# Kernel tuning notes

Hardware: AMD Instinct MI355X
Metric: run time of the kernel (lower is better)

## Reference

```python
import jax, jax.numpy as jnp
import jax.scipy.linalg as jsl
import numpy as np

B, T, C = 2, 4096, 1024
HK = HV = 8           # linear_num_key_heads == linear_num_value_heads
DK = DV = 128         # linear_key_head_dim / linear_value_head_dim
CHUNK = 64
CONV_K = 4
KEY_DIM = HK * DK
VAL_DIM = HV * DV
CONV_DIM = 2 * KEY_DIM + VAL_DIM
EPS = 1e-6


def setup_inputs() -> dict:
    key = jax.random.key(0)
    ks = jax.random.split(key, 8)
    s = 0.02
    x = jax.random.normal(ks[0], (B, T, C), jnp.float32)
    W_qkvz = jax.random.normal(ks[1], (C, 2 * KEY_DIM + 2 * VAL_DIM), jnp.float32) * s
    W_ba = jax.random.normal(ks[2], (C, 2 * HV), jnp.float32) * s
    conv_w = jax.random.normal(ks[3], (CONV_DIM, 1, CONV_K), jnp.float32) * 0.3  # depthwise (O,1,K)
    dt_bias = jnp.ones((HV,), jnp.float32)
    A_log = jnp.log(jax.random.uniform(ks[4], (HV,), jnp.float32, 0.5, 8.0))
    norm_weight = jnp.ones((DV,), jnp.float32)
    W_out = jax.random.normal(ks[5], (VAL_DIM, C), jnp.float32) * s
    return {"x": x, "W_qkvz": W_qkvz, "W_ba": W_ba, "conv_w": conv_w,
            "dt_bias": dt_bias, "A_log": A_log, "norm_weight": norm_weight, "W_out": W_out}


def _l2norm(x, eps=EPS):
    return x * jax.lax.rsqrt(jnp.sum(x * x, -1, keepdims=True) + eps)


def _chunk_gated_delta_rule(q, k, v, g, beta, chunk=CHUNK):
    # q,k: (B,T,H,DK); v: (B,T,H,DV); g,beta: (B,T,H)
    q = _l2norm(q)
    k = _l2norm(k)
    tr = lambda x: jnp.swapaxes(x, 1, 2).astype(jnp.float32)  # -> (B,H,T,...)
    q, k, v, g, beta = tr(q), tr(k), tr(v), tr(g), tr(beta)
    b, h, t, dk = k.shape
    dv = v.shape[-1]
    n = t // chunk  # T divisible by chunk (pad_size == 0)
    q = q * (dk ** -0.5)
    v_beta = v * beta[..., None]
    k_beta = k * beta[..., None]
    rs = lambda x: x.reshape(b, h, n, chunk, x.shape[-1])
    q, k, v_beta, k_beta = rs(q), rs(k), rs(v_beta), rs(k_beta)
    g = jnp.cumsum(g.reshape(b, h, n, chunk), axis=-1)
    # decay_mask[..., i, j] = exp(g_i - g_j) for j <= i, else 0
    decay = jnp.tril(jnp.exp(jnp.tril(g[..., :, None] - g[..., None, :])))
    # forward substitution == unit-lower-triangular solve: (I + tri)^{-1}
    tri = jnp.tril(jnp.einsum('bhnck,bhndk->bhncd', k_beta, k) * decay, -1)
    eye = jnp.eye(chunk, dtype=jnp.float32)
    Tm = jsl.solve_triangular(eye + tri, jnp.broadcast_to(eye, tri.shape), lower=True)
    v_new = Tm @ v_beta                                   # (B,H,N,C,DV)
    k_cum = Tm @ (k_beta * jnp.exp(g)[..., None])         # (B,H,N,C,DK)
    keep_low = jnp.tril(jnp.ones((chunk, chunk), bool))

    def step(S, inp):
        q_i, k_i, v_i, kc_i, g_i, dm_i = inp              # (B,H,C,*)
        attn = jnp.where(keep_low, (q_i @ jnp.swapaxes(k_i, -1, -2)) * dm_i, 0.0)
        v_n = v_i - kc_i @ S
        out = (q_i * jnp.exp(g_i)[..., None]) @ S + attn @ v_n
        g_last = g_i[..., -1]
        S = S * jnp.exp(g_last)[..., None, None] + jnp.einsum(
            'bhck,bhcv->bhkv', k_i * jnp.exp(g_last[..., None] - g_i)[..., None], v_n)
        return S, out

    mv = lambda x: jnp.moveaxis(x, 2, 0)                  # chunk axis to front
    S0 = jnp.zeros((b, h, dk, dv), jnp.float32)
    S, outs = jax.lax.scan(step, S0, (mv(q), mv(k), mv(v_new), mv(k_cum), mv(g), mv(decay)))
    out = jnp.moveaxis(outs, 0, 2).reshape(b, h, t, dv)
    return jnp.swapaxes(out, 1, 2), S                     # (B,T,H,DV), (B,H,DK,DV)


def reference(x, W_qkvz, W_ba, conv_w, dt_bias, A_log, norm_weight, W_out):
    Bx, Tx, Cx = x.shape
    ratio = HV // HK
    qkvz = (x @ W_qkvz).reshape(Bx, Tx, HK, 2 * DK + 2 * ratio * DV)
    q, k, v, z = jnp.split(qkvz, [DK, 2 * DK, 2 * DK + ratio * DV], axis=3)
    v = v.reshape(Bx, Tx, HV, DV)
    z = z.reshape(Bx, Tx, HV, DV)
    ba = (x @ W_ba).reshape(Bx, Tx, HK, 2 * ratio)
    b_, a_ = jnp.split(ba, [ratio], axis=3)
    b_ = b_.reshape(Bx, Tx, HV)
    a_ = a_.reshape(Bx, Tx, HV)
    mixed = jnp.concatenate([q.reshape(Bx, Tx, -1), k.reshape(Bx, Tx, -1),
                             v.reshape(Bx, Tx, -1)], axis=-1)
    # causal depthwise conv1d (left pad K-1, take first T)
    xc = jnp.swapaxes(mixed, 1, 2)                        # (B, CONV_DIM, T)
    conv = jax.lax.conv_general_dilated(xc, conv_w, (1,), [(CONV_K - 1, 0)],
                                        dimension_numbers=('NCH', 'OIH', 'NCH'),
                                        feature_group_count=CONV_DIM)
    conv = jnp.swapaxes(jax.nn.silu(conv), 1, 2)          # (B,T,CONV_DIM)
    qc, kc, vc = jnp.split(conv, [KEY_DIM, 2 * KEY_DIM], axis=-1)
    qc = qc.reshape(Bx, Tx, HK, DK)
    kc = kc.reshape(Bx, Tx, HK, DK)
    vc = vc.reshape(Bx, Tx, HV, DV)
    if ratio > 1:
        qc = jnp.repeat(qc, ratio, axis=2)
        kc = jnp.repeat(kc, ratio, axis=2)
    beta = jax.nn.sigmoid(b_)
    g = -jnp.exp(A_log) * jax.nn.softplus(a_ + dt_bias)
    core, _ = _chunk_gated_delta_rule(qc, kc, vc, g, beta)
    # GatedRMSNorm over head_v_dim, gated by silu(z)
    h = core.astype(jnp.float32)
    var = jnp.mean(h * h, -1, keepdims=True)
    h = norm_weight * (h * jax.lax.rsqrt(var + EPS))
    h = h * jax.nn.silu(z.astype(jnp.float32))
    return h.reshape(Bx, Tx, VAL_DIM) @ W_out
```

## Files before the change

kernel.cpp:

```cpp
#include <hip/hip_runtime.h>
#include <cstddef>

#define Bx 2
#define Tn 4096
#define Hh 8

typedef unsigned short u16;
typedef unsigned int u32;
typedef __attribute__((ext_vector_type(8))) short short8;
typedef __attribute__((ext_vector_type(4))) float f32x4;

__device__ __forceinline__ float bf2f(u16 u) {
  u32 x = ((u32)u) << 16;
  return __uint_as_float(x);
}
__device__ __forceinline__ u16 f2bf(float f) {
  u32 x = __float_as_uint(f);
  u32 lsb = (x >> 16) & 1;
  x += 0x7fffu + lsb;
  return (u16)(x >> 16);
}
__device__ __forceinline__ u32 pack2(float a, float b) {
  return (u32)f2bf(a) | ((u32)f2bf(b) << 16);
}
__device__ __forceinline__ short8 cvt8(float4 f0, float4 f1) {
  uint4 p;
  p.x = pack2(f0.x, f0.y);
  p.y = pack2(f0.z, f0.w);
  p.z = pack2(f1.x, f1.y);
  p.w = pack2(f1.z, f1.w);
  return *(short8*)&p;
}
__device__ __forceinline__ void async16(u16* lds, const u16* g) {
  __builtin_amdgcn_global_load_lds((const __attribute__((address_space(1))) void*)g,
                                   (__attribute__((address_space(3))) void*)lds, 16, 0, 0);
}

__global__ __launch_bounds__(256) void conv_bf16(const float* __restrict__ X,
                                                 u16* __restrict__ Xb) {
  int i = (blockIdx.x * 256 + threadIdx.x) * 8;
  float4 v0 = *(const float4*)&X[i];
  float4 v1 = *(const float4*)&X[i + 4];
  uint4 pv;
  pv.x = pack2(v0.x, v0.y);
  pv.y = pack2(v0.z, v0.w);
  pv.z = pack2(v1.x, v1.y);
  pv.w = pack2(v1.z, v1.w);
  *(uint4*)&Xb[i] = pv;
}

__global__ __launch_bounds__(256) void transpose_bf16(const float* __restrict__ W,
                                                      u16* __restrict__ WT,
                                                      int K, int N) {
  __shared__ float tile[64][68];
  int nb = blockIdx.x, kb = blockIdx.y;
  int tid = threadIdx.x;
  int r = tid >> 4, c4 = (tid & 15) * 4;
#pragma unroll
  for (int p = 0; p < 4; p++) {
    int k = kb * 64 + p * 16 + r;
    float4 v = *(const float4*)&W[(size_t)k * N + nb * 64 + c4];
    tile[p * 16 + r][c4] = v.x;
    tile[p * 16 + r][c4 + 1] = v.y;
    tile[p * 16 + r][c4 + 2] = v.z;
    tile[p * 16 + r][c4 + 3] = v.w;
  }
  __syncthreads();
  int rn = tid >> 2, ck = (tid & 3) * 16;
#pragma unroll
  for (int s = 0; s < 2; s++) {
    int k0 = ck + s * 8;
    uint4 pv;
    pv.x = pack2(tile[k0 + 0][rn], tile[k0 + 1][rn]);
    pv.y = pack2(tile[k0 + 2][rn], tile[k0 + 3][rn]);
    pv.z = pack2(tile[k0 + 4][rn], tile[k0 + 5][rn]);
    pv.w = pack2(tile[k0 + 6][rn], tile[k0 + 7][rn]);
    *(uint4*)&WT[(size_t)(nb * 64 + rn) * K + kb * 64 + k0] = pv;
  }
}

template<int EPI>
__global__ __launch_bounds__(256) void gemm_mfma(const u16* __restrict__ A,
                                                 const u16* __restrict__ Bt,
                                                 u16* __restrict__ O1,
                                                 u16* __restrict__ O2,
                                                 float* __restrict__ O3,
                                                 int Nfull) {
  const int K = 1024;
  __shared__ u16 As[128 * 32];
  __shared__ u16 Bs[128 * 32];
  int bn = blockIdx.x, bm = blockIdx.y;
  int tid = threadIdx.x;
  int wave = tid >> 6, lane = tid & 63;
  int wr = wave >> 1, wc = wave & 1;

  f32x4 acc[4][4];
#pragma unroll
  for (int i = 0; i < 4; i++)
#pragma unroll
    for (int j = 0; j < 4; j++) acc[i][j] = (f32x4){0.f, 0.f, 0.f, 0.f};

  const u16* Ab = A + (size_t)(bm * 128 + wave * 32 + (lane >> 2)) * K + (lane & 3) * 8;
  const u16* Bb = Bt + (size_t)(bn * 128 + wave * 32 + (lane >> 2)) * K + (lane & 3) * 8;
  u16* AsW = &As[(wave * 32) * 32];
  u16* BsW = &Bs[(wave * 32) * 32];

  int m_lane = lane & 15, k_lane = (lane >> 4) * 8;
  const u16* arow0 = &As[(wr * 64 + m_lane) * 32 + k_lane];
  const u16* brow0 = &Bs[(wc * 64 + m_lane) * 32 + k_lane];

  for (int kk = 0; kk < K; kk += 32) {
    __syncthreads();
    async16(AsW, Ab + kk);
    async16(AsW + 16 * 32, Ab + 16 * K + kk);
    async16(BsW, Bb + kk);
    async16(BsW + 16 * 32, Bb + 16 * K + kk);
    __syncthreads();
    short8 a[4], b[4];
#pragma unroll
    for (int t = 0; t < 4; t++) a[t] = *(const short8*)(arow0 + t * 16 * 32);
#pragma unroll
    for (int t = 0; t < 4; t++) b[t] = *(const short8*)(brow0 + t * 16 * 32);
#pragma unroll
    for (int i = 0; i < 4; i++)
#pragma unroll
      for (int j = 0; j < 4; j++)
        acc[i][j] = __builtin_amdgcn_mfma_f32_16x16x32_bf16(a[i], b[j], acc[i][j], 0, 0, 0);
  }

  int n0 = bn * 128;
  int cbase = wc * 64 + (lane & 15);
  int rbase = bm * 128 + wr * 64 + ((lane >> 4) * 4);
  if (EPI == 1) {
    int h = n0 >> 9, sub = (n0 >> 7) & 3;
    u16* dst;
    size_t stride;
    if (sub < 3) { dst = O1 + (size_t)(sub * 1024 + h * 128); stride = 3072; }
    else         { dst = O2 + (size_t)(h * 128);              stride = 1024; }
#pragma unroll
    for (int i = 0; i < 4; i++)
#pragma unroll
      for (int j = 0; j < 4; j++)
#pragma unroll
        for (int r = 0; r < 4; r++)
          dst[(size_t)(rbase + i * 16 + r) * stride + cbase + j * 16] = f2bf(acc[i][j][r]);
  } else {
#pragma unroll
    for (int i = 0; i < 4; i++)
#pragma unroll
      for (int j = 0; j < 4; j++)
#pragma unroll
        for (int r = 0; r < 4; r++)
          O3[(size_t)(rbase + i * 16 + r) * Nfull + n0 + cbase + j * 16] = acc[i][j][r];
  }
}

__global__ __launch_bounds__(128) void ba_kernel(const float* __restrict__ x,
                                                 const float* __restrict__ Wba,
                                                 const float* __restrict__ dtb,
                                                 const float* __restrict__ Alog,
                                                 float* __restrict__ betab,
                                                 float* __restrict__ gb) {
  __shared__ float xs[1024];
  __shared__ float part[8][16];
  int row = blockIdx.x, tid = threadIdx.x;
#pragma unroll
  for (int r = 0; r < 2; r++) {
    int f4 = r * 128 + tid;
    *(float4*)&xs[f4 * 4] = *(const float4*)&x[(size_t)row * 1024 + f4 * 4];
  }
  __syncthreads();
  int col = tid & 15, seg = tid >> 4;
  float a = 0.f;
  for (int k = seg * 128; k < seg * 128 + 128; k++) a += xs[k] * Wba[k * 16 + col];
  part[seg][col] = a;
  __syncthreads();
  if (tid < 8) {
    float bval = 0.f, aval = 0.f;
#pragma unroll
    for (int q = 0; q < 8; q++) { bval += part[q][tid * 2]; aval += part[q][tid * 2 + 1]; }
    betab[(size_t)row * 8 + tid] = 1.f / (1.f + expf(-bval));
    float spin = aval + dtb[tid];
    float sp = (spin > 20.f) ? spin : log1pf(expf(spin));
    gb[(size_t)row * 8 + tid] = -expf(Alog[tid]) * sp;
  }
}

__global__ __launch_bounds__(256) void convnorm(const u16* __restrict__ mixed,
                                                const float* __restrict__ cw,
                                                const float* __restrict__ gbuf,
                                                u16* __restrict__ qn,
                                                u16* __restrict__ kn,
                                                u16* __restrict__ kdT) {
  __shared__ __align__(16) u16 sRaw[67 * 128];
  __shared__ __align__(16) u16 sO[64 * 136];
  __shared__ float red_s[256];
  __shared__ float inv_s[64];
  __shared__ float eglc_s[64];
  int n = blockIdx.x, bh = blockIdx.y, type = blockIdx.z;
  int b = bh >> 3, h = bh & 7;
  int t0 = n * 64, tid = threadIdx.x;
  int srow = tid >> 4, scol8 = (tid & 15) * 8;
  int base = type * 1024;

#pragma unroll
  for (int pass = 0; pass < 5; pass++) {
    int r = pass * 16 + srow;
    if (r < 67) {
      int t = t0 - 3 + r;
      uint4 v = make_uint4(0u, 0u, 0u, 0u);
      if (t >= 0) v = *(const uint4*)&mixed[(size_t)(b * Tn + t) * 3072 + base + h * 128 + scol8];
      *(uint4*)&sRaw[r * 128 + scol8] = v;
    }
  }
  if (type == 1 && tid < 64) {
    float gv = gbuf[(size_t)(b * Tn + t0 + tid) * 8 + h];
#pragma unroll
    for (int off = 1; off < 64; off <<= 1) {
      float o = __shfl_up(gv, off, 64);
      if (tid >= off) gv += o;
    }
    float gl = __shfl(gv, 63, 64);
    eglc_s[tid] = expf(gl - gv);
  }
  __syncthreads();

#pragma unroll
  for (int it = 0; it < 32; it++) {
    int idx = it * 256 + tid;
    int i = idx >> 7, d = idx & 127;
    int colw = (base + h * 128 + d) * 4;
    float a = 0.f;
#pragma unroll
    for (int tap = 0; tap < 4; tap++)
      a += bf2f(sRaw[(i + tap) * 128 + d]) * cw[colw + tap];
    a = a / (1.f + expf(-a));
    sO[i * 136 + d] = f2bf(a);
  }
  __syncthreads();
  {
    int i = tid >> 2, p = tid & 3;
    float ss = 0.f;
#pragma unroll
    for (int d = p * 32; d < p * 32 + 32; d += 2) {
      u32 w2 = *(const u32*)&sO[i * 136 + d];
      float a = bf2f(w2 & 0xffff), b2 = bf2f(w2 >> 16);
      ss += a * a + b2 * b2;
    }
    red_s[tid] = ss;
  }
  __syncthreads();
  if (tid < 64) {
    float inv = rsqrtf(red_s[tid * 4] + red_s[tid * 4 + 1] + red_s[tid * 4 + 2] + red_s[tid * 4 + 3] + 1e-6f);
    inv_s[tid] = (type == 0) ? inv * 0.08838834764831845f : inv;
  }
  __syncthreads();
  u16* dstRow = (type == 0 ? qn : kn) + (size_t)(bh * Tn + t0) * 128;
#pragma unroll
  for (int it = 0; it < 16; it++) {
    int idx = it * 256 + tid;
    int i = idx >> 6, d2 = (idx & 63) * 2;
    u32 w2 = *(const u32*)&sO[i * 136 + d2];
    float inv = inv_s[i];
    float q0 = bf2f(w2 & 0xffff) * inv, q1 = bf2f(w2 >> 16) * inv;
    u32 pk = pack2(q0, q1);
    if (type == 1) *(u32*)&sO[i * 136 + d2] = pk;
    *(u32*)&dstRow[(size_t)i * 128 + d2] = pk;
  }
  if (type == 1) {
    __syncthreads();
    const size_t tbase = (size_t)(bh * 64 + n) * 8192;
#pragma unroll
    for (int it = 0; it < 32; it++) {
      int idx = it * 256 + tid;
      int d = idx >> 6, i = idx & 63;
      kdT[tbase + d * 64 + i] = f2bf(bf2f(sO[i * 136 + d]) * eglc_s[i]);
    }
  }
}

__global__ __launch_bounds__(256) void prep(const u16* __restrict__ mixed,
                                            const float* __restrict__ cw,
                                            const float* __restrict__ gbuf,
                                            const float* __restrict__ betabuf,
                                            u16* qbuf,
                                            u16* kbuf,
                                            u16* __restrict__ vnT,
                                            u16* __restrict__ attn,
                                            float* __restrict__ egl) {
  __shared__ __align__(16) u16 sKn[64 * 136];
  __shared__ __align__(16) u16 sQn[64 * 136];
  __shared__ __align__(16) u16 sRawV[67 * 128];
  __shared__ float gc_s[64], egc_s[64], bet_s[64];
  float* triL = (float*)sQn;

  int n = blockIdx.x, bh = blockIdx.y;
  int b = bh >> 3, h = bh & 7;
  int t0 = n * 64;
  int tid = threadIdx.x;
  const int rowg0 = b * Tn + t0;
  const int rowh0 = bh * Tn + t0;
  const size_t tbase = (size_t)(bh * 64 + n) * 8192;

  int wv = tid >> 6, lane = tid & 63;
  int m16 = lane & 15, q8 = (lane >> 4) * 8, qr = (lane >> 4) * 4;
  int srow = tid >> 4, scol8 = (tid & 15) * 8;

#pragma unroll
  for (int it = 0; it < 4; it++) {
    int idx = it * 256 + tid;
    int i = idx >> 4, c8 = (idx & 15) * 8;
    *(uint4*)&sQn[i * 136 + c8] = *(const uint4*)&qbuf[(size_t)(rowh0 + i) * 128 + c8];
    *(uint4*)&sKn[i * 136 + c8] = *(const uint4*)&kbuf[(size_t)(rowh0 + i) * 128 + c8];
  }
#pragma unroll
  for (int pass = 0; pass < 5; pass++) {
    int r = pass * 16 + srow;
    if (r < 67) {
      int t = t0 - 3 + r;
      uint4 v = make_uint4(0u, 0u, 0u, 0u);
      if (t >= 0) v = *(const uint4*)&mixed[(size_t)(b * Tn + t) * 3072 + 2048 + h * 128 + scol8];
      *(uint4*)&sRawV[r * 128 + scol8] = v;
    }
  }
  if (tid < 64) {
    float gv = gbuf[(size_t)(rowg0 + tid) * 8 + h];
    float bv = betabuf[(size_t)(rowg0 + tid) * 8 + h];
#pragma unroll
    for (int off = 1; off < 64; off <<= 1) {
      float o = __shfl_up(gv, off, 64);
      if (tid >= off) gv += o;
    }
    float gl = __shfl(gv, 63, 64);
    gc_s[tid] = gv;
    egc_s[tid] = expf(gv);
    bet_s[tid] = bv;
    if (tid == 63) egl[bh * 64 + n] = expf(gl);
  }
  __syncthreads();

#pragma unroll
  for (int it = 0; it < 16; it++) {
    int idx = it * 256 + tid;
    int i = idx >> 6, d2 = (idx & 63) * 2;
    u32 w2 = *(const u32*)&sQn[i * 136 + d2];
    float e = egc_s[i];
    *(u32*)&qbuf[(size_t)(rowh0 + i) * 128 + d2] =
        pack2(bf2f(w2 & 0xffff) * e, bf2f(w2 >> 16) * e);
  }
  {
    short8 qa[4];
#pragma unroll
    for (int kt = 0; kt < 4; kt++)
      qa[kt] = *(const short8*)&sQn[(wv * 16 + m16) * 136 + kt * 32 + q8];
    u16* atp = attn + (size_t)(bh * 64 + n) * 4096;
#pragma unroll
    for (int jt = 0; jt < 4; jt++) {
      int j = jt * 16 + m16;
      if (jt <= wv) {
        f32x4 o = (f32x4){0.f, 0.f, 0.f, 0.f};
#pragma unroll
        for (int kt = 0; kt < 4; kt++) {
          short8 kb = *(const short8*)&sKn[(jt * 16 + m16) * 136 + kt * 32 + q8];
          o = __builtin_amdgcn_mfma_f32_16x16x32_bf16(qa[kt], kb, o, 0, 0, 0);
        }
#pragma unroll
        for (int r = 0; r < 4; r++) {
          int i = wv * 16 + qr + r;
          float val = (j <= i) ? o[r] * expf(gc_s[i] - gc_s[j]) : 0.f;
          atp[i * 64 + j] = f2bf(val);
        }
      } else {
#pragma unroll
        for (int r = 0; r < 4; r++) atp[(wv * 16 + qr + r) * 64 + j] = 0;
      }
    }
  }
  __syncthreads();
  {
    short8 ka[4];
#pragma unroll
    for (int kt = 0; kt < 4; kt++)
      ka[kt] = *(const short8*)&sKn[(wv * 16 + m16) * 136 + kt * 32 + q8];
#pragma unroll
    for (int jt = 0; jt < 4; jt++) {
      int j = jt * 16 + m16;
      if (jt <= wv) {
        f32x4 o = (f32x4){0.f, 0.f, 0.f, 0.f};
#pragma unroll
        for (int kt = 0; kt < 4; kt++) {
          short8 kb = *(const short8*)&sKn[(jt * 16 + m16) * 136 + kt * 32 + q8];
          o = __builtin_amdgcn_mfma_f32_16x16x32_bf16(ka[kt], kb, o, 0, 0, 0);
        }
#pragma unroll
        for (int r = 0; r < 4; r++) {
          int i = wv * 16 + qr + r;
          triL[i * 64 + j] = (j < i) ? bet_s[i] * expf(gc_s[i] - gc_s[j]) * o[r] : 0.f;
        }
      } else if (jt == wv + 1) {
#pragma unroll
        for (int r = 0; r < 4; r++) triL[(wv * 16 + qr + r) * 64 + j] = 0.f;
      }
    }
  }
  __syncthreads();

  {
    int mat = tid >> 7, c = tid & 127;
    float x[64];
    if (mat == 0) {
#pragma unroll
      for (int i = 0; i < 64; i++)
        x[i] = bf2f(sKn[i * 136 + c]) * bet_s[i] * egc_s[i];
    } else {
      float cwv[4];
      int colw = (2048 + h * 128 + c) * 4;
#pragma unroll
      for (int tap = 0; tap < 4; tap++) cwv[tap] = cw[colw + tap];
#pragma unroll
      for (int i = 0; i < 64; i++) {
        float a = 0.f;
#pragma unroll
        for (int tap = 0; tap < 4; tap++)
          a += bf2f(sRawV[(i + tap) * 128 + c]) * cwv[tap];
        a = a / (1.f + expf(-a));
        x[i] = a * bet_s[i];
      }
    }
#pragma unroll
    for (int i = 1; i < 64; i++) {
      float s0 = 0.f, s1 = 0.f, s2 = 0.f, s3 = 0.f;
#pragma unroll
      for (int l4 = 0; l4 < (i + 3) / 4; l4++) {
        float4 t4 = *(float4*)&triL[i * 64 + l4 * 4];
        s0 += t4.x * x[l4 * 4 + 0];
        s1 += t4.y * x[l4 * 4 + 1];
        s2 += t4.z * x[l4 * 4 + 2];
        s3 += t4.w * x[l4 * 4 + 3];
      }
      x[i] = x[i] - ((s0 + s1) + (s2 + s3));
    }
    if (mat == 0) {
#pragma unroll
      for (int i = 0; i < 64; i++) kbuf[(size_t)(rowh0 + i) * 128 + c] = f2bf(-x[i]);
    } else {
#pragma unroll
      for (int i = 0; i < 64; i += 2)
        *(u32*)&vnT[tbase + c * 64 + i] = pack2(x[i], x[i + 1]);
    }
  }
}

__device__ __forceinline__ void stage_scan(u16* ldsb,
                                           const u16* __restrict__ qgc,
                                           const u16* __restrict__ kcc,
                                           const u16* __restrict__ ktc,
                                           const u16* __restrict__ atc,
                                           const u16* __restrict__ vtc,
                                           int lane) {
  int l8 = lane * 8;
#pragma unroll
  for (int i = 0; i < 16; i++) {
    int p = i * 512 + l8;
    async16(ldsb + i * 512, qgc + (p ^ ((((p >> 7) & 15)) << 3)));
  }
#pragma unroll
  for (int i = 0; i < 16; i++) {
    int p = i * 512 + l8;
    async16(ldsb + 8192 + i * 512, kcc + (p ^ ((((p >> 7) & 15)) << 3)));
  }
#pragma unroll
  for (int i = 0; i < 16; i++) {
    int p = i * 512 + l8;
    async16(ldsb + 16384 + i * 512, ktc + (p ^ ((((p >> 6) & 7)) << 3)));
  }
#pragma unroll
  for (int i = 0; i < 8; i++) {
    int p = i * 512 + l8;
    async16(ldsb + 24576 + i * 512, atc + (p ^ ((((p >> 6) & 7)) << 3)));
  }
#pragma unroll
  for (int i = 0; i < 2; i++) {
    int p = i * 512 + l8;
    async16(ldsb + 28672 + i * 512, vtc + (p ^ ((((p >> 6) & 7)) << 3)));
  }
}

__global__ __launch_bounds__(64, 1) void scan_mfma(const u16* __restrict__ qg,
                                                   const u16* __restrict__ kdT,
                                                   const u16* __restrict__ vnT,
                                                   const u16* __restrict__ kcum,
                                                   const u16* __restrict__ attn,
                                                   const float* __restrict__ egl,
                                                   float* __restrict__ core) {
  extern __shared__ __align__(16) u16 dyn[];
  __shared__ float ST[16 * 132];
  __shared__ float VN[16 * 68];
  int blk = blockIdx.x;
  int bh = blk & 15, tile = blk >> 4;
  int dv0 = tile * 16;
  int b = bh >> 3, h = bh & 7;
  int lane = threadIdx.x;
  int q = lane >> 4, col = lane & 15;
  int c7 = col & 7;

  for (int r = lane; r < 16 * 132; r += 64) ST[r] = 0.f;
  float egAll = egl[bh * 64 + lane];

  const u16* qg_base = qg + (size_t)bh * Tn * 128;
  const u16* kc_base = kcum + (size_t)bh * Tn * 128;
  const u16* kt_base = kdT + (size_t)bh * 64 * 8192;
  const u16* at_base = attn + (size_t)bh * 64 * 4096;
  const u16* vt_base = vnT + (size_t)bh * 64 * 8192 + dv0 * 64;

  stage_scan(dyn, qg_base, kc_base, kt_base, at_base, vt_base, lane);
  asm volatile("s_waitcnt vmcnt(0)" ::: "memory");

  for (int n = 0; n < 64; n++) {
    u16* buf = dyn + (n & 1) * 29696;

    short8 kcf[16], qgf[16], ktf[16], atf[8];
    uint2 vtf[4];
#pragma unroll
    for (int mt = 0; mt < 4; mt++) {
#pragma unroll
      for (int kt = 0; kt < 4; kt++) {
        kcf[mt * 4 + kt] = *(const short8*)&buf[8192 + (mt * 16 + col) * 128 +
                                                (((kt * 4 + q) ^ col) << 3)];
        qgf[mt * 4 + kt] = *(const short8*)&buf[(mt * 16 + col) * 128 +
                                                (((kt * 4 + q) ^ col) << 3)];
      }
#pragma unroll
      for (int kt2 = 0; kt2 < 2; kt2++)
        atf[mt * 2 + kt2] = *(const short8*)&buf[24576 + (mt * 16 + col) * 64 +
                                                 (((kt2 * 4 + q) ^ c7) << 3)];
      vtf[mt] = *(const uint2*)&buf[28672 + col * 64 +
                                    (((mt * 2 + (q >> 1)) ^ c7) << 3) + (q & 1) * 4];
    }
#pragma unroll
    for (int t = 0; t < 8; t++)
#pragma unroll
      for (int kt2 = 0; kt2 < 2; kt2++)
        ktf[t * 2 + kt2] = *(const short8*)&buf[16384 + (t * 16 + col) * 64 +
                                                (((kt2 * 4 + q) ^ c7) << 3)];
    short8 sb[4];
#pragma unroll
    for (int kt = 0; kt < 4; kt++) {
      float4 f0 = *(float4*)&ST[col * 132 + kt * 32 + q * 8];
      float4 f1 = *(float4*)&ST[col * 132 + kt * 32 + q * 8 + 4];
      sb[kt] = cvt8(f0, f1);
    }
    float4 stu[8];
#pragma unroll
    for (int t = 0; t < 8; t++) stu[t] = *(float4*)&ST[col * 132 + t * 16 + q * 4];

    if (n < 63) {
      stage_scan(dyn + ((n + 1) & 1) * 29696,
                 qg_base + (size_t)(n + 1) * 8192,
                 kc_base + (size_t)(n + 1) * 8192,
                 kt_base + (size_t)(n + 1) * 8192,
                 at_base + (size_t)(n + 1) * 4096,
                 vt_base + (size_t)(n + 1) * 8192, lane);
    }
    float eg = __shfl(egAll, n, 64);

    f32x4 vn[4];
#pragma unroll
    for (int mt = 0; mt < 4; mt++) {
      f32x4 a0;
      a0[0] = bf2f(vtf[mt].x & 0xffff); a0[1] = bf2f(vtf[mt].x >> 16);
      a0[2] = bf2f(vtf[mt].y & 0xffff); a0[3] = bf2f(vtf[mt].y >> 16);
#pragma unroll
      for (int kt = 0; kt < 4; kt++)
        a0 = __builtin_amdgcn_mfma_f32_16x16x32_bf16(kcf[mt * 4 + kt], sb[kt], a0, 0, 0, 0);
      vn[mt] = a0;
    }
#pragma unroll
    for (int mt = 0; mt < 4; mt++)
      *(f32x4*)&VN[col * 68 + mt * 16 + q * 4] = vn[mt];
    short8 vb[2];
#pragma unroll
    for (int kt2 = 0; kt2 < 2; kt2++) {
      float4 f0 = *(float4*)&VN[col * 68 + kt2 * 32 + q * 8];
      float4 f1 = *(float4*)&VN[col * 68 + kt2 * 32 + q * 8 + 4];
      vb[kt2] = cvt8(f0, f1);
    }

#pragma unroll
    for (int t = 0; t < 8; t++) {
      f32x4 s0;
      s0[0] = stu[t].x * eg; s0[1] = stu[t].y * eg;
      s0[2] = stu[t].z * eg; s0[3] = stu[t].w * eg;
#pragma unroll
      for (int kt2 = 0; kt2 < 2; kt2++)
        s0 = __builtin_amdgcn_mfma_f32_16x16x32_bf16(ktf[t * 2 + kt2], vb[kt2], s0, 0, 0, 0);
      *(f32x4*)&ST[col * 132 + t * 16 + q * 4] = s0;
    }

#pragma unroll
    for (int mt = 0; mt < 4; mt++) {
      f32x4 o = (f32x4){0.f, 0.f, 0.f, 0.f};
#pragma unroll
      for (int kt = 0; kt < 4; kt++)
        o = __builtin_amdgcn_mfma_f32_16x16x32_bf16(qgf[mt * 4 + kt], sb[kt], o, 0, 0, 0);
#pragma unroll
      for (int kt2 = 0; kt2 < 2; kt2++)
        o = __builtin_amdgcn_mfma_f32_16x16x32_bf16(atf[mt * 2 + kt2], vb[kt2], o, 0, 0, 0);
      size_t rowb = (size_t)(b * Tn) + n * 64 + mt * 16 + q * 4;
#pragma unroll
      for (int r2 = 0; r2 < 4; r2++)
        core[(rowb + r2) * 1024 + h * 128 + dv0 + col] = o[r2];
    }

    asm volatile("s_waitcnt vmcnt(0)" ::: "memory");
  }
}

__global__ __launch_bounds__(256) void gnorm(const float* __restrict__ core,
                                             const u16* __restrict__ z,
                                             const float* __restrict__ nw,
                                             u16* __restrict__ coreb) {
  __shared__ float red[256];
  __shared__ float rstd[8];
  int row = blockIdx.x, tid = threadIdx.x;
  float4 c4 = *(const float4*)&core[(size_t)row * 1024 + tid * 4];
  uint2 zl = *(const uint2*)&z[(size_t)row * 1024 + tid * 4];
  float4 z4;
  z4.x = bf2f(zl.x & 0xffff); z4.y = bf2f(zl.x >> 16);
  z4.z = bf2f(zl.y & 0xffff); z4.w = bf2f(zl.y >> 16);
  red[tid] = c4.x * c4.x + c4.y * c4.y + c4.z * c4.z + c4.w * c4.w;
  __syncthreads();
  if (tid < 8) {
    float s = 0.f;
    for (int t2 = tid * 32; t2 < tid * 32 + 32; t2++) s += red[t2];
    rstd[tid] = rsqrtf(s * (1.f / 128.f) + 1e-6f);
  }
  __syncthreads();
  float rs = rstd[tid >> 5];
  int d0 = (tid * 4) & 127;
  float4 w4 = *(const float4*)&nw[d0];
  float4 o;
  o.x = c4.x * rs * w4.x * (z4.x / (1.f + expf(-z4.x)));
  o.y = c4.y * rs * w4.y * (z4.y / (1.f + expf(-z4.y)));
  o.z = c4.z * rs * w4.z * (z4.z / (1.f + expf(-z4.z)));
  o.w = c4.w * rs * w4.w * (z4.w / (1.f + expf(-z4.w)));
  uint2 pv;
  pv.x = pack2(o.x, o.y);
  pv.y = pack2(o.z, o.w);
  *(uint2*)&coreb[(size_t)row * 1024 + tid * 4] = pv;
}

extern "C" void kernel_launch(void* const* d_in, const int* in_sizes, int n_in,
                              void* d_out, int out_size, void* d_ws, size_t ws_size,
                              hipStream_t stream) {
  const float* x     = (const float*)d_in[0];
  const float* Wqkvz = (const float*)d_in[1];
  const float* Wba   = (const float*)d_in[2];
  const float* convw = (const float*)d_in[3];
  const float* dtb   = (const float*)d_in[4];
  const float* Alog  = (const float*)d_in[5];
  const float* nw    = (const float*)d_in[6];
  const float* Wout  = (const float*)d_in[7];
  float* out = (float*)d_out;

  char* w = (char*)d_ws;
  u16*   mixed = (u16*)w;
  float* core  = (float*)w;
  u16*   coreb = (u16*)(w + 33554432);
  u16*   zb    = (u16*)(w + 50331648);
  float* betab = (float*)(w + 67108864);
  float* gb    = (float*)(w + 67371008);
  u16*   qgB   = (u16*)(w + 67633152);
  u16*   xb    = (u16*)(w + 67633152);
  u16*   kdTB  = (u16*)(w + 84410368);
  u16*   WqT   = (u16*)(w + 84410368);
  u16*   vnTB  = (u16*)(w + 101187584);
  u16*   kcB   = (u16*)(w + 117964800);
  u16*   WoT   = (u16*)(w + 117964800);
  u16*   atB   = (u16*)(w + 134742016);
  float* eglB  = (float*)(w + 143130624);

  static bool attr_set = false;
  if (!attr_set) {
    hipFuncSetAttribute(reinterpret_cast<const void*>(scan_mfma),
                        hipFuncAttributeMaxDynamicSharedMemorySize, 118784);
    attr_set = true;
  }

  conv_bf16<<<dim3(4096), 256, 0, stream>>>(x, xb);
  transpose_bf16<<<dim3(64, 16), 256, 0, stream>>>(Wqkvz, WqT, 1024, 4096);
  gemm_mfma<1><<<dim3(32, 64), 256, 0, stream>>>(xb, WqT, mixed, zb, nullptr, 4096);
  ba_kernel<<<dim3(8192), 128, 0, stream>>>(x, Wba, dtb, Alog, betab, gb);
  convnorm<<<dim3(64, 16, 2), 256, 0, stream>>>(mixed, convw, gb, qgB, kcB, kdTB);
  prep<<<dim3(64, 16), 256, 0, stream>>>(mixed, convw, gb, betab, qgB, kcB, vnTB, atB, eglB);
  scan_mfma<<<dim3(128), 64, 118784, stream>>>(qgB, kdTB, vnTB, kcB, atB, eglB, core);
  transpose_bf16<<<dim3(16, 16), 256, 0, stream>>>(Wout, WoT, 1024, 1024);
  gnorm<<<dim3(8192), 256, 0, stream>>>(core, zb, nw, coreb);
  gemm_mfma<0><<<dim3(8, 64), 256, 0, stream>>>(coreb, WoT, nullptr, nullptr, out, 1024);
}
```

Before: 470.0 us.

## Split scan chunk work across two waves per block with barrier sync

The recurrent scan kernel goes from one wave per block to two. Each wave now takes half of the row tiles for the output and VN products and half of the state tiles for the state update. Each wave also loads its own half of the next chunk's operands asynchronously. LDS barriers are added so the VN intermediate and the state are complete before either wave reads them, and the end-of-iteration wait now skips the just-issued global stores. This is meant to cut the serial per-chunk latency of the scan, at the cost of two block-wide barriers per chunk.

```diff
diff --git a/kernel.cpp b/kernel.cpp
--- a/kernel.cpp
+++ b/kernel.cpp
@@ -451,7 +451,7 @@
   }
 }
 
-__device__ __forceinline__ void stage_scan(u16* ldsb,
+__device__ __forceinline__ void stage_half(int w, u16* ldsb,
                                            const u16* __restrict__ qgc,
                                            const u16* __restrict__ kcc,
                                            const u16* __restrict__ ktc,
@@ -459,40 +459,43 @@
                                            const u16* __restrict__ vtc,
                                            int lane) {
   int l8 = lane * 8;
-#pragma unroll
-  for (int i = 0; i < 16; i++) {
-    int p = i * 512 + l8;
-    async16(ldsb + i * 512, qgc + (p ^ ((((p >> 7) & 15)) << 3)));
-  }
-#pragma unroll
-  for (int i = 0; i < 16; i++) {
-    int p = i * 512 + l8;
-    async16(ldsb + 8192 + i * 512, kcc + (p ^ ((((p >> 7) & 15)) << 3)));
-  }
-#pragma unroll
-  for (int i = 0; i < 16; i++) {
-    int p = i * 512 + l8;
-    async16(ldsb + 16384 + i * 512, ktc + (p ^ ((((p >> 6) & 7)) << 3)));
-  }
-#pragma unroll
-  for (int i = 0; i < 8; i++) {
-    int p = i * 512 + l8;
-    async16(ldsb + 24576 + i * 512, atc + (p ^ ((((p >> 6) & 7)) << 3)));
-  }
-#pragma unroll
-  for (int i = 0; i < 2; i++) {
-    int p = i * 512 + l8;
-    async16(ldsb + 28672 + i * 512, vtc + (p ^ ((((p >> 6) & 7)) << 3)));
-  }
-}
-
-__global__ __launch_bounds__(64, 1) void scan_mfma(const u16* __restrict__ qg,
-                                                   const u16* __restrict__ kdT,
-                                                   const u16* __restrict__ vnT,
-                                                   const u16* __restrict__ kcum,
-                                                   const u16* __restrict__ attn,
-                                                   const float* __restrict__ egl,
-                                                   float* __restrict__ core) {
+  if (w == 0) {
+#pragma unroll
+    for (int i = 0; i < 16; i++) {
+      int p = i * 512 + l8;
+      async16(ldsb + i * 512, qgc + (p ^ ((((p >> 7) & 15)) << 3)));
+    }
+#pragma unroll
+    for (int i = 0; i < 8; i++) {
+      int p = i * 512 + l8;
+      async16(ldsb + 24576 + i * 512, atc + (p ^ ((((p >> 6) & 7)) << 3)));
+    }
+#pragma unroll
+    for (int i = 0; i < 2; i++) {
+      int p = i * 512 + l8;
+      async16(ldsb + 28672 + i * 512, vtc + (p ^ ((((p >> 6) & 7)) << 3)));
+    }
+  } else {
+#pragma unroll
+    for (int i = 0; i < 16; i++) {
+      int p = i * 512 + l8;
+      async16(ldsb + 8192 + i * 512, kcc + (p ^ ((((p >> 7) & 15)) << 3)));
+    }
+#pragma unroll
+    for (int i = 0; i < 16; i++) {
+      int p = i * 512 + l8;
+      async16(ldsb + 16384 + i * 512, ktc + (p ^ ((((p >> 6) & 7)) << 3)));
+    }
+  }
+}
+
+__global__ __launch_bounds__(128, 1) void scan_mfma(const u16* __restrict__ qg,
+                                                    const u16* __restrict__ kdT,
+                                                    const u16* __restrict__ vnT,
+                                                    const u16* __restrict__ kcum,
+                                                    const u16* __restrict__ attn,
+                                                    const float* __restrict__ egl,
+                                                    float* __restrict__ core) {
   extern __shared__ __align__(16) u16 dyn[];
   __shared__ float ST[16 * 132];
   __shared__ float VN[16 * 68];
@@ -500,11 +503,13 @@
   int bh = blk & 15, tile = blk >> 4;
   int dv0 = tile * 16;
   int b = bh >> 3, h = bh & 7;
-  int lane = threadIdx.x;
+  int tid = threadIdx.x;
+  int w = tid >> 6, lane = tid & 63;
   int q = lane >> 4, col = lane & 15;
   int c7 = col & 7;
-
-  for (int r = lane; r < 16 * 132; r += 64) ST[r] = 0.f;
+  int tw0 = w * 4;
+
+  for (int r = tid; r < 16 * 132; r += 128) ST[r] = 0.f;
   float egAll = egl[bh * 64 + lane];
 
   const u16* qg_base = qg + (size_t)bh * Tn * 128;
@@ -513,35 +518,37 @@
   const u16* at_base = attn + (size_t)bh * 64 * 4096;
   const u16* vt_base = vnT + (size_t)bh * 64 * 8192 + dv0 * 64;
 
-  stage_scan(dyn, qg_base, kc_base, kt_base, at_base, vt_base, lane);
+  stage_half(w, dyn, qg_base, kc_base, kt_base, at_base, vt_base, lane);
   asm volatile("s_waitcnt vmcnt(0)" ::: "memory");
+  __syncthreads();
 
   for (int n = 0; n < 64; n++) {
     u16* buf = dyn + (n & 1) * 29696;
 
-    short8 kcf[16], qgf[16], ktf[16], atf[8];
-    uint2 vtf[4];
-#pragma unroll
-    for (int mt = 0; mt < 4; mt++) {
+    short8 kcf[8], qgf[8], ktf[8], atf[4];
+    uint2 vtf[2];
+#pragma unroll
+    for (int m = 0; m < 2; m++) {
+      int mt = w * 2 + m;
 #pragma unroll
       for (int kt = 0; kt < 4; kt++) {
-        kcf[mt * 4 + kt] = *(const short8*)&buf[8192 + (mt * 16 + col) * 128 +
-                                                (((kt * 4 + q) ^ col) << 3)];
-        qgf[mt * 4 + kt] = *(const short8*)&buf[(mt * 16 + col) * 128 +
-                                                (((kt * 4 + q) ^ col) << 3)];
+        kcf[m * 4 + kt] = *(const short8*)&buf[8192 + (mt * 16 + col) * 128 +
+                                               (((kt * 4 + q) ^ col) << 3)];
+        qgf[m * 4 + kt] = *(const short8*)&buf[(mt * 16 + col) * 128 +
+                                               (((kt * 4 + q) ^ col) << 3)];
       }
 #pragma unroll
       for (int kt2 = 0; kt2 < 2; kt2++)
-        atf[mt * 2 + kt2] = *(const short8*)&buf[24576 + (mt * 16 + col) * 64 +
-                                                 (((kt2 * 4 + q) ^ c7) << 3)];
-      vtf[mt] = *(const uint2*)&buf[28672 + col * 64 +
-                                    (((mt * 2 + (q >> 1)) ^ c7) << 3) + (q & 1) * 4];
-    }
-#pragma unroll
-    for (int t = 0; t < 8; t++)
+        atf[m * 2 + kt2] = *(const short8*)&buf[24576 + (mt * 16 + col) * 64 +
+                                                (((kt2 * 4 + q) ^ c7) << 3)];
+      vtf[m] = *(const uint2*)&buf[28672 + col * 64 +
+                                   (((mt * 2 + (q >> 1)) ^ c7) << 3) + (q & 1) * 4];
+    }
+#pragma unroll
+    for (int t = 0; t < 4; t++)
 #pragma unroll
       for (int kt2 = 0; kt2 < 2; kt2++)
-        ktf[t * 2 + kt2] = *(const short8*)&buf[16384 + (t * 16 + col) * 64 +
+        ktf[t * 2 + kt2] = *(const short8*)&buf[16384 + ((tw0 + t) * 16 + col) * 64 +
                                                 (((kt2 * 4 + q) ^ c7) << 3)];
     short8 sb[4];
 #pragma unroll
@@ -550,12 +557,12 @@
       float4 f1 = *(float4*)&ST[col * 132 + kt * 32 + q * 8 + 4];
       sb[kt] = cvt8(f0, f1);
     }
-    float4 stu[8];
-#pragma unroll
-    for (int t = 0; t < 8; t++) stu[t] = *(float4*)&ST[col * 132 + t * 16 + q * 4];
+    float4 stu[4];
+#pragma unroll
+    for (int t = 0; t < 4; t++) stu[t] = *(float4*)&ST[col * 132 + (tw0 + t) * 16 + q * 4];
 
     if (n < 63) {
-      stage_scan(dyn + ((n + 1) & 1) * 29696,
+      stage_half(w, dyn + ((n + 1) & 1) * 29696,
                  qg_base + (size_t)(n + 1) * 8192,
                  kc_base + (size_t)(n + 1) * 8192,
                  kt_base + (size_t)(n + 1) * 8192,
@@ -564,20 +571,20 @@
     }
     float eg = __shfl(egAll, n, 64);
 
-    f32x4 vn[4];
-#pragma unroll
-    for (int mt = 0; mt < 4; mt++) {
+#pragma unroll
+    for (int m = 0; m < 2; m++) {
       f32x4 a0;
-      a0[0] = bf2f(vtf[mt].x & 0xffff); a0[1] = bf2f(vtf[mt].x >> 16);
-      a0[2] = bf2f(vtf[mt].y & 0xffff); a0[3] = bf2f(vtf[mt].y >> 16);
+      a0[0] = bf2f(vtf[m].x & 0xffff); a0[1] = bf2f(vtf[m].x >> 16);
+      a0[2] = bf2f(vtf[m].y & 0xffff); a0[3] = bf2f(vtf[m].y >> 16);
 #pragma unroll
       for (int kt = 0; kt < 4; kt++)
-        a0 = __builtin_amdgcn_mfma_f32_16x16x32_bf16(kcf[mt * 4 + kt], sb[kt], a0, 0, 0, 0);
-      vn[mt] = a0;
-    }
-#pragma unroll
-    for (int mt = 0; mt < 4; mt++)
-      *(f32x4*)&VN[col * 68 + mt * 16 + q * 4] = vn[mt];
+        a0 = __builtin_amdgcn_mfma_f32_16x16x32_bf16(kcf[m * 4 + kt], sb[kt], a0, 0, 0, 0);
+      *(f32x4*)&VN[col * 68 + (w * 2 + m) * 16 + q * 4] = a0;
+    }
+    asm volatile("s_waitcnt lgkmcnt(0)" ::: "memory");
+    __builtin_amdgcn_s_barrier();
+    __builtin_amdgcn_sched_barrier(0);
+
     short8 vb[2];
 #pragma unroll
     for (int kt2 = 0; kt2 < 2; kt2++) {
@@ -587,32 +594,34 @@
     }
 
 #pragma unroll
-    for (int t = 0; t < 8; t++) {
+    for (int t = 0; t < 4; t++) {
       f32x4 s0;
       s0[0] = stu[t].x * eg; s0[1] = stu[t].y * eg;
       s0[2] = stu[t].z * eg; s0[3] = stu[t].w * eg;
 #pragma unroll
       for (int kt2 = 0; kt2 < 2; kt2++)
         s0 = __builtin_amdgcn_mfma_f32_16x16x32_bf16(ktf[t * 2 + kt2], vb[kt2], s0, 0, 0, 0);
-      *(f32x4*)&ST[col * 132 + t * 16 + q * 4] = s0;
-    }
-
-#pragma unroll
-    for (int mt = 0; mt < 4; mt++) {
+      *(f32x4*)&ST[col * 132 + (tw0 + t) * 16 + q * 4] = s0;
+    }
+
+#pragma unroll
+    for (int m = 0; m < 2; m++) {
       f32x4 o = (f32x4){0.f, 0.f, 0.f, 0.f};
 #pragma unroll
       for (int kt = 0; kt < 4; kt++)
-        o = __builtin_amdgcn_mfma_f32_16x16x32_bf16(qgf[mt * 4 + kt], sb[kt], o, 0, 0, 0);
+        o = __builtin_amdgcn_mfma_f32_16x16x32_bf16(qgf[m * 4 + kt], sb[kt], o, 0, 0, 0);
 #pragma unroll
       for (int kt2 = 0; kt2 < 2; kt2++)
-        o = __builtin_amdgcn_mfma_f32_16x16x32_bf16(atf[mt * 2 + kt2], vb[kt2], o, 0, 0, 0);
-      size_t rowb = (size_t)(b * Tn) + n * 64 + mt * 16 + q * 4;
+        o = __builtin_amdgcn_mfma_f32_16x16x32_bf16(atf[m * 2 + kt2], vb[kt2], o, 0, 0, 0);
+      size_t rowb = (size_t)(b * Tn) + n * 64 + (w * 2 + m) * 16 + q * 4;
 #pragma unroll
       for (int r2 = 0; r2 < 4; r2++)
         core[(rowb + r2) * 1024 + h * 128 + dv0 + col] = o[r2];
     }
 
-    asm volatile("s_waitcnt vmcnt(0)" ::: "memory");
+    asm volatile("s_waitcnt vmcnt(8) lgkmcnt(0)" ::: "memory");
+    __builtin_amdgcn_s_barrier();
+    __builtin_amdgcn_sched_barrier(0);
   }
 }
 
@@ -693,7 +702,7 @@
   ba_kernel<<<dim3(8192), 128, 0, stream>>>(x, Wba, dtb, Alog, betab, gb);
   convnorm<<<dim3(64, 16, 2), 256, 0, stream>>>(mixed, convw, gb, qgB, kcB, kdTB);
   prep<<<dim3(64, 16), 256, 0, stream>>>(mixed, convw, gb, betab, qgB, kcB, vnTB, atB, eglB);
-  scan_mfma<<<dim3(128), 64, 118784, stream>>>(qgB, kdTB, vnTB, kcB, atB, eglB, core);
+  scan_mfma<<<dim3(128), 128, 118784, stream>>>(qgB, kdTB, vnTB, kcB, atB, eglB, core);
   transpose_bf16<<<dim3(16, 16), 256, 0, stream>>>(Wout, WoT, 1024, 1024);
   gnorm<<<dim3(8192), 256, 0, stream>>>(core, zb, nw, coreb);
   gemm_mfma<0><<<dim3(8, 64), 256, 0, stream>>>(coreb, WoT, nullptr, nullptr, out, 1024);
```

Measured after the change: 446.3 us. -5.0%, faster.
